# Kernel tuning notes

Measured on AMD Instinct MI355X. Metric: run time of the kernel, lower is better.

The kernel has to match this reference:

```python
import jax, jax.numpy as jnp
import numpy as np

N_NODES = 100000
N_EDGES = 1600000
IN_DIM, HID_DIM, OUT_DIM = 128, 256, 1


def setup_inputs() -> dict:
    key = jax.random.key(0)
    ks = jax.random.split(key, 8)
    x = jax.random.normal(ks[0], (N_NODES, IN_DIM), dtype=jnp.float32)
    edge_index = jax.random.randint(ks[1], (2, N_EDGES), 0, N_NODES, dtype=jnp.int64)
    # Glorot-ish scaled params (values arbitrary; shapes match GCNConv/Linear)
    W1 = jax.random.normal(ks[2], (IN_DIM, HID_DIM), dtype=jnp.float32) / np.sqrt(IN_DIM)
    b1 = jnp.zeros((HID_DIM,), dtype=jnp.float32)
    W2 = jax.random.normal(ks[3], (HID_DIM, HID_DIM), dtype=jnp.float32) / np.sqrt(HID_DIM)
    b2 = jnp.zeros((HID_DIM,), dtype=jnp.float32)
    Wout = jax.random.normal(ks[4], (HID_DIM, OUT_DIM), dtype=jnp.float32) / np.sqrt(HID_DIM)
    bout = jnp.zeros((OUT_DIM,), dtype=jnp.float32)
    return {"x": x, "edge_index": edge_index, "W1": W1, "b1": b1,
            "W2": W2, "b2": b2, "Wout": Wout, "bout": bout}


def _gcn_norm(edge_index, num_nodes):
    # add self loops, compute symmetric normalization deg^-1/2[src]*deg^-1/2[dst]
    loops = jnp.arange(num_nodes, dtype=edge_index.dtype)
    src = jnp.concatenate([edge_index[0], loops])
    dst = jnp.concatenate([edge_index[1], loops])
    deg = jax.ops.segment_sum(jnp.ones_like(dst, dtype=jnp.float32), dst,
                              num_segments=num_nodes)
    dinv = jnp.where(deg > 0, jax.lax.rsqrt(deg), 0.0)
    norm = dinv[src] * dinv[dst]  # [E + N]
    return src, dst, norm


def _gcn_layer(x, src, dst, norm, W, b, num_nodes):
    h = x @ W                                   # [N, F_out] dense transform
    msg = h[src] * norm[:, None]                # gather + scale  [E', F_out]
    agg = jax.ops.segment_sum(msg, dst, num_segments=num_nodes)  # scatter-add
    return agg + b


def reference(x, edge_index, W1, b1, W2, b2, Wout, bout):
    n = x.shape[0]
    src, dst, norm = _gcn_norm(edge_index, n)
    h = jax.nn.relu(_gcn_layer(x, src, dst, norm, W1, b1, n))
    h = jax.nn.relu(_gcn_layer(h, src, dst, norm, W2, b2, n))
    pooled = jnp.mean(h, axis=0, keepdims=True)  # global_mean_pool, one graph -> [1, H]
    return pooled @ Wout + bout                  # [1, 1]
```

## Files before the change

kernel.cpp:

```cpp
#include <hip/hip_runtime.h>
#include <hip/hip_bf16.h>


typedef __attribute__((ext_vector_type(8))) short short8;
typedef __attribute__((ext_vector_type(4))) float f32x4;
typedef __attribute__((ext_vector_type(2))) float f32x2;

#define BKT_SHIFT 9
#define BKT_NODES 512
#define BIN_CHUNK 8192
#define CAP 10240

__device__ inline unsigned short f2bf(float f) {
    union { float f; unsigned u; } v; v.f = f;
    unsigned r = (v.u + 0x7fff + ((v.u >> 16) & 1)) >> 16;
    return (unsigned short)r;
}

__global__ void init_k(int* __restrict__ bcur, float* __restrict__ pool, int NB) {
    int t = blockIdx.x * 256 + threadIdx.x;
    if (t < NB) bcur[t] = t * CAP;
    if (t < 256) pool[t] = 0.f;
}

__global__ __launch_bounds__(256) void bin_k(const int* __restrict__ ei,
                                             int* __restrict__ bcur,
                                             uint2* __restrict__ pairs,
                                             int E, int N, int NB) {
    __shared__ int hist[256];
    __shared__ int base[256];
    int chunk0 = blockIdx.x * BIN_CHUNK;
    for (int t = threadIdx.x; t < NB; t += 256) hist[t] = 0;
    __syncthreads();
#pragma unroll 4
    for (int i = 0; i < BIN_CHUNK / 256; ++i) {
        int e = chunk0 + i * 256 + threadIdx.x;
        if (e < E) {
            unsigned d = (unsigned)ei[(size_t)E + e];
            if (d < (unsigned)N) atomicAdd(&hist[d >> BKT_SHIFT], 1);
        }
    }
    __syncthreads();
    for (int t = threadIdx.x; t < NB; t += 256) {
        int c = hist[t];
        base[t] = c ? atomicAdd(&bcur[t], c) : 0;
        hist[t] = 0;
    }
    __syncthreads();
#pragma unroll 4
    for (int i = 0; i < BIN_CHUNK / 256; ++i) {
        int e = chunk0 + i * 256 + threadIdx.x;
        if (e < E) {
            unsigned d = (unsigned)ei[(size_t)E + e];
            unsigned s = (unsigned)ei[e];
            if (d < (unsigned)N) {
                int b = d >> BKT_SHIFT;
                int r = atomicAdd(&hist[b], 1);
                unsigned sc = (s < (unsigned)N) ? s : 0u;
                pairs[base[b] + r] = make_uint2(sc, d);
            }
        }
    }
}

__global__ __launch_bounds__(512) void scatter_k(const uint2* __restrict__ pairs,
                                                 const int* __restrict__ bcur,
                                                 int* __restrict__ off,
                                                 int* __restrict__ deg,
                                                 float* __restrict__ dinv,
                                                 int* __restrict__ csr, int N) {
    __shared__ int h[2][512];
    __shared__ int cur[512];
    int b = blockIdx.x, t = threadIdx.x;
    int lo = b << BKT_SHIFT;
    int rs = b * CAP;
    int re = min(bcur[b], rs + CAP);
    h[0][t] = 0;
    __syncthreads();
    for (int i = rs + t; i < re; i += 512)
        atomicAdd(&h[0][pairs[i].y - lo], 1);
    __syncthreads();
    int v = h[0][t];
    int cu = 0;
    for (int o = 1; o < 512; o <<= 1) {
        int val = h[cu][t];
        if (t >= o) val += h[cu][t - o];
        h[cu ^ 1][t] = val;
        cu ^= 1;
        __syncthreads();
    }
    int no = rs + (h[cu][t] - v);
    if (lo + t < N) {
        off[lo + t] = no;
        deg[lo + t] = v;
        dinv[lo + t] = rsqrtf((float)v + 1.0f);
    }
    cur[t] = no;
    __syncthreads();
    for (int i = rs + t; i < re; i += 512) {
        uint2 p = pairs[i];
        int pos = atomicAdd(&cur[p.y - lo], 1);
        csr[pos] = (int)p.x;
    }
}

__global__ void cvtx_k(const float* __restrict__ x, const float* __restrict__ dinv,
                       unsigned* __restrict__ Xs, int n32) {
    int idx = blockIdx.x * 256 + threadIdx.x;
    if (idx >= n32) return;
    int i = idx >> 5;
    float4 v = ((const float4*)x)[idx];
    float di = dinv[i];
    float a = fminf(fmaxf(di * v.x, -448.f), 448.f);
    float b = fminf(fmaxf(di * v.y, -448.f), 448.f);
    float c = fminf(fmaxf(di * v.z, -448.f), 448.f);
    float d = fminf(fmaxf(di * v.w, -448.f), 448.f);
    int p = __builtin_amdgcn_cvt_pk_fp8_f32(a, b, 0, false);
    p = __builtin_amdgcn_cvt_pk_fp8_f32(c, d, p, true);
    Xs[idx] = (unsigned)p;
}

__global__ void wt_k(const float* __restrict__ W, unsigned short* __restrict__ Wt, int K) {
    int idx = blockIdx.x * 256 + threadIdx.x;
    if (idx >= K * 256) return;
    int k = idx >> 8, nn = idx & 255;
    Wt[nn * K + k] = f2bf(W[idx]);
}

__global__ __launch_bounds__(256) void agg128_k(const unsigned short* __restrict__ X8,
                                                const int* __restrict__ csr,
                                                const int* __restrict__ off,
                                                const int* __restrict__ deg,
                                                const float* __restrict__ dinv,
                                                unsigned short* __restrict__ O8, int n) {
    int w = (blockIdx.x * 256 + threadIdx.x) >> 6;
    int lane = threadIdx.x & 63;
    if (w >= n) return;
    int st = off[w], c = deg[w];
    float di = dinv[w];
    f32x2 sv = __builtin_amdgcn_cvt_pk_f32_fp8((int)X8[(size_t)w * 64 + lane], false);
    float ax[4], ay[4];
    ax[0] = sv[0]; ay[0] = sv[1];
    ax[1] = ax[2] = ax[3] = 0.f; ay[1] = ay[2] = ay[3] = 0.f;
    int e = 0;
    for (; e + 8 <= c; e += 8) {
        int s[8];
#pragma unroll
        for (int j = 0; j < 8; ++j) s[j] = csr[st + e + j];
        unsigned short u[8];
#pragma unroll
        for (int j = 0; j < 8; ++j) u[j] = X8[(size_t)s[j] * 64 + lane];
#pragma unroll
        for (int j = 0; j < 8; ++j) {
            f32x2 f = __builtin_amdgcn_cvt_pk_f32_fp8((int)u[j], false);
            ax[j & 3] += f[0]; ay[j & 3] += f[1];
        }
    }
    if (e + 4 <= c) {
        int s[4];
#pragma unroll
        for (int j = 0; j < 4; ++j) s[j] = csr[st + e + j];
        unsigned short u[4];
#pragma unroll
        for (int j = 0; j < 4; ++j) u[j] = X8[(size_t)s[j] * 64 + lane];
#pragma unroll
        for (int j = 0; j < 4; ++j) {
            f32x2 f = __builtin_amdgcn_cvt_pk_f32_fp8((int)u[j], false);
            ax[j] += f[0]; ay[j] += f[1];
        }
        e += 4;
    }
    for (; e < c; ++e) {
        int s = csr[st + e];
        f32x2 f = __builtin_amdgcn_cvt_pk_f32_fp8((int)X8[(size_t)s * 64 + lane], false);
        ax[0] += f[0]; ay[0] += f[1];
    }
    float ox = di * ((ax[0] + ax[1]) + (ax[2] + ax[3]));
    float oy = di * ((ay[0] + ay[1]) + (ay[2] + ay[3]));
    ox = fminf(fmaxf(ox, -448.f), 448.f);
    oy = fminf(fmaxf(oy, -448.f), 448.f);
    int pk = __builtin_amdgcn_cvt_pk_fp8_f32(ox, oy, 0, false);
    O8[(size_t)w * 64 + lane] = (unsigned short)(pk & 0xffff);
}

__global__ __launch_bounds__(256) void agg256_k(const unsigned* __restrict__ H8,
                                                const int* __restrict__ csr,
                                                const int* __restrict__ off,
                                                const int* __restrict__ deg,
                                                const float* __restrict__ dinv,
                                                unsigned* __restrict__ O8, int n) {
    int w = (blockIdx.x * 256 + threadIdx.x) >> 6;
    int lane = threadIdx.x & 63;
    if (w >= n) return;
    int st = off[w], c = deg[w];
    float di = dinv[w];
    unsigned su = H8[(size_t)w * 64 + lane];
    f32x2 slo = __builtin_amdgcn_cvt_pk_f32_fp8((int)su, false);
    f32x2 shi = __builtin_amdgcn_cvt_pk_f32_fp8((int)su, true);
    float a[4][4];
    a[0][0] = slo[0]; a[0][1] = slo[1]; a[0][2] = shi[0]; a[0][3] = shi[1];
#pragma unroll
    for (int g = 1; g < 4; ++g) { a[g][0] = a[g][1] = a[g][2] = a[g][3] = 0.f; }
    int e = 0;
    for (; e + 8 <= c; e += 8) {
        int s[8];
#pragma unroll
        for (int j = 0; j < 8; ++j) s[j] = csr[st + e + j];
        unsigned u[8];
#pragma unroll
        for (int j = 0; j < 8; ++j) u[j] = H8[(size_t)s[j] * 64 + lane];
#pragma unroll
        for (int j = 0; j < 8; ++j) {
            f32x2 lo = __builtin_amdgcn_cvt_pk_f32_fp8((int)u[j], false);
            f32x2 hi = __builtin_amdgcn_cvt_pk_f32_fp8((int)u[j], true);
            a[j & 3][0] += lo[0]; a[j & 3][1] += lo[1];
            a[j & 3][2] += hi[0]; a[j & 3][3] += hi[1];
        }
    }
    if (e + 4 <= c) {
        int s[4];
#pragma unroll
        for (int j = 0; j < 4; ++j) s[j] = csr[st + e + j];
        unsigned u[4];
#pragma unroll
        for (int j = 0; j < 4; ++j) u[j] = H8[(size_t)s[j] * 64 + lane];
#pragma unroll
        for (int j = 0; j < 4; ++j) {
            f32x2 lo = __builtin_amdgcn_cvt_pk_f32_fp8((int)u[j], false);
            f32x2 hi = __builtin_amdgcn_cvt_pk_f32_fp8((int)u[j], true);
            a[j][0] += lo[0]; a[j][1] += lo[1]; a[j][2] += hi[0]; a[j][3] += hi[1];
        }
        e += 4;
    }
    for (; e < c; ++e) {
        int s = csr[st + e];
        unsigned u = H8[(size_t)s * 64 + lane];
        f32x2 lo = __builtin_amdgcn_cvt_pk_f32_fp8((int)u, false);
        f32x2 hi = __builtin_amdgcn_cvt_pk_f32_fp8((int)u, true);
        a[0][0] += lo[0]; a[0][1] += lo[1]; a[0][2] += hi[0]; a[0][3] += hi[1];
    }
    float o0 = di * ((a[0][0] + a[1][0]) + (a[2][0] + a[3][0]));
    float o1 = di * ((a[0][1] + a[1][1]) + (a[2][1] + a[3][1]));
    float o2 = di * ((a[0][2] + a[1][2]) + (a[2][2] + a[3][2]));
    float o3 = di * ((a[0][3] + a[1][3]) + (a[2][3] + a[3][3]));
    o0 = fminf(fmaxf(o0, -448.f), 448.f);
    o1 = fminf(fmaxf(o1, -448.f), 448.f);
    o2 = fminf(fmaxf(o2, -448.f), 448.f);
    o3 = fminf(fmaxf(o3, -448.f), 448.f);
    int pk = __builtin_amdgcn_cvt_pk_fp8_f32(o0, o1, 0, false);
    pk = __builtin_amdgcn_cvt_pk_fp8_f32(o2, o3, pk, true);
    O8[(size_t)w * 64 + lane] = (unsigned)pk;
}

template <int MODE>
__global__ __launch_bounds__(256) void mgemm_k(const unsigned char* __restrict__ A8,
                                               const unsigned short* __restrict__ Bt,
                                               const float* __restrict__ bias,
                                               const float* __restrict__ dinv,
                                               unsigned char* __restrict__ Hout8,
                                               float* __restrict__ pool,
                                               int M, int K) {
    __shared__ __align__(16) short As[64 * 40];
    __shared__ __align__(16) short Bs[256 * 40];
    int tid = threadIdx.x;
    int w = tid >> 6, lane = tid & 63, lr = lane >> 4, lc = lane & 15;
    int row0 = blockIdx.x * 64;
    int arow = tid >> 2, akoff = (tid & 3) * 8;
    f32x4 acc[16] = {};

    for (int kt = 0; kt < K; kt += 32) {
        short8 va = {};
        int gr = row0 + arow;
        if (gr < M) {
            uint2 v = *(const uint2*)(A8 + (size_t)gr * K + kt + akoff);
            f32x2 f0 = __builtin_amdgcn_cvt_pk_f32_fp8((int)v.x, false);
            f32x2 f1 = __builtin_amdgcn_cvt_pk_f32_fp8((int)v.x, true);
            f32x2 f2 = __builtin_amdgcn_cvt_pk_f32_fp8((int)v.y, false);
            f32x2 f3 = __builtin_amdgcn_cvt_pk_f32_fp8((int)v.y, true);
            va[0] = (short)f2bf(f0[0]); va[1] = (short)f2bf(f0[1]);
            va[2] = (short)f2bf(f1[0]); va[3] = (short)f2bf(f1[1]);
            va[4] = (short)f2bf(f2[0]); va[5] = (short)f2bf(f2[1]);
            va[6] = (short)f2bf(f3[0]); va[7] = (short)f2bf(f3[1]);
        }
        *(short8*)&As[arow * 40 + akoff] = va;
#pragma unroll
        for (int l = 0; l < 4; ++l) {
            int f = tid + l * 256;
            int br = f >> 2, bk = (f & 3) * 8;
            short8 vb = *(const short8*)(Bt + (size_t)br * K + kt + bk);
            *(short8*)&Bs[br * 40 + bk] = vb;
        }
        __syncthreads();
        short8 af = *(const short8*)&As[(w * 16 + lc) * 40 + lr * 8];
#pragma unroll
        for (int f = 0; f < 16; ++f) {
            short8 bf = *(const short8*)&Bs[(f * 16 + lc) * 40 + lr * 8];
            acc[f] = __builtin_amdgcn_mfma_f32_16x16x32_bf16(af, bf, acc[f], 0, 0, 0);
        }
        __syncthreads();
    }

    float bv[16];
#pragma unroll
    for (int f = 0; f < 16; ++f) bv[f] = bias[f * 16 + lc];

    if (MODE == 1) {
#pragma unroll
        for (int r = 0; r < 4; ++r) {
            int gr = row0 + w * 16 + lr * 4 + r;
            if (gr < M) {
                float dr = dinv[gr];
#pragma unroll
                for (int f = 0; f < 16; ++f) {
                    float v = fminf(dr * fmaxf(acc[f][r] + bv[f], 0.f), 448.f);
                    int p = __builtin_amdgcn_cvt_pk_fp8_f32(v, v, 0, false);
                    Hout8[(size_t)gr * 256 + f * 16 + lc] = (unsigned char)(p & 0xff);
                }
            }
        }
    } else {
        __shared__ float red[16][256];
        float s[16];
#pragma unroll
        for (int f = 0; f < 16; ++f) s[f] = 0.f;
#pragma unroll
        for (int r = 0; r < 4; ++r) {
            int gr = row0 + w * 16 + lr * 4 + r;
            if (gr < M) {
#pragma unroll
                for (int f = 0; f < 16; ++f)
                    s[f] += fmaxf(acc[f][r] + bv[f], 0.f);
            }
        }
#pragma unroll
        for (int f = 0; f < 16; ++f) red[w * 4 + lr][f * 16 + lc] = s[f];
        __syncthreads();
        float t = 0.f;
#pragma unroll
        for (int rr = 0; rr < 16; ++rr) t += red[rr][tid];
        atomicAdd(&pool[tid], t);
    }
}

__global__ void final_k(const float* __restrict__ pool, const float* __restrict__ Wout,
                        const float* __restrict__ bout, float* __restrict__ out, float invM) {
    __shared__ float s[256];
    int t = threadIdx.x;
    s[t] = pool[t] * invM * Wout[t];
    __syncthreads();
    for (int o = 128; o > 0; o >>= 1) {
        if (t < o) s[t] += s[t + o];
        __syncthreads();
    }
    if (t == 0) out[0] = s[0] + bout[0];
}

extern "C" void kernel_launch(void* const* d_in, const int* in_sizes, int n_in,
                              void* d_out, int out_size, void* d_ws, size_t ws_size,
                              hipStream_t stream) {
    const float* x    = (const float*)d_in[0];
    const int*   ei   = (const int*)d_in[1];
    const float* W1   = (const float*)d_in[2];
    const float* b1   = (const float*)d_in[3];
    const float* W2   = (const float*)d_in[4];
    const float* b2   = (const float*)d_in[5];
    const float* Wout = (const float*)d_in[6];
    const float* bout = (const float*)d_in[7];
    float* out = (float*)d_out;

    const int N = in_sizes[0] / 128;
    const int E = in_sizes[1] / 2;
    const int NB = (N + BKT_NODES - 1) / BKT_NODES;

    char* p = (char*)d_ws;
    auto carve = [&](size_t bytes) -> void* {
        void* r = (void*)p;
        p += (bytes + 511) & ~(size_t)511;
        return r;
    };
    unsigned*       Xs   = (unsigned*)carve((size_t)N * 128);
    unsigned short* Xp   = (unsigned short*)carve((size_t)N * 128);
    unsigned char*  H1   = (unsigned char*)carve((size_t)N * 256);
    unsigned*       G    = (unsigned*)carve((size_t)N * 256);
    unsigned short* Wt1  = (unsigned short*)carve((size_t)128 * 256 * 2);
    unsigned short* Wt2  = (unsigned short*)carve((size_t)256 * 256 * 2);
    float* dinv   = (float*)carve((size_t)N * 4);
    int*   off    = (int*)carve((size_t)N * 4);
    int*   deg    = (int*)carve((size_t)N * 4);
    int*   csr    = (int*)carve((size_t)NB * CAP * 4);
    uint2* pairs  = (uint2*)carve((size_t)NB * CAP * 8);
    int*   bcur   = (int*)carve((size_t)NB * 4);
    float* pool   = (float*)carve(256 * 4);

    init_k<<<1, 256, 0, stream>>>(bcur, pool, NB);
    bin_k<<<(E + BIN_CHUNK - 1) / BIN_CHUNK, 256, 0, stream>>>(ei, bcur, pairs, E, N, NB);
    scatter_k<<<NB, 512, 0, stream>>>(pairs, bcur, off, deg, dinv, csr, N);

    cvtx_k<<<(N * 32 + 255) / 256, 256, 0, stream>>>(x, dinv, Xs, N * 32);
    wt_k<<<(128 * 256 + 255) / 256, 256, 0, stream>>>(W1, Wt1, 128);
    wt_k<<<(256 * 256 + 255) / 256, 256, 0, stream>>>(W2, Wt2, 256);

    agg128_k<<<(N + 3) / 4, 256, 0, stream>>>((const unsigned short*)Xs, csr, off, deg, dinv, Xp, N);
    mgemm_k<1><<<(N + 63) / 64, 256, 0, stream>>>(
        (const unsigned char*)Xp, Wt1, b1, dinv, H1, nullptr, N, 128);

    agg256_k<<<(N + 3) / 4, 256, 0, stream>>>((const unsigned*)H1, csr, off, deg, dinv, G, N);
    mgemm_k<2><<<(N + 63) / 64, 256, 0, stream>>>(
        (const unsigned char*)G, Wt2, b2, nullptr, nullptr, pool, N, 256);

    final_k<<<1, 256, 0, stream>>>(pool, Wout, bout, out, 1.0f / N);
}
```

Measured before the change: 279.5 us.

## Fuse edge binning, x conversion and weight transposes into one prep kernel

Edge binning, fp8 conversion of x and both weight transposes now run as one multi-role kernel. To allow this, the x conversion no longer applies dinv, since dinv is only known after scatter. Instead the first aggregation multiplies each gathered neighbor by its own dinv, which adds a per-edge scalar gather. The bucket size is halved to 256 nodes with a smaller capacity, giving more scatter blocks, and init_k is replaced by memsets. This removes launches and the serial dependency of the conversion on scatter, at the cost of extra per-edge loads and fp8 quantization of unscaled x.

```diff
diff --git a/kernel.cpp b/kernel.cpp
--- a/kernel.cpp
+++ b/kernel.cpp
@@ -6,10 +6,10 @@
 typedef __attribute__((ext_vector_type(4))) float f32x4;
 typedef __attribute__((ext_vector_type(2))) float f32x2;
 
-#define BKT_SHIFT 9
-#define BKT_NODES 512
+#define BKT_SHIFT 8
+#define BKT_NODES 256
 #define BIN_CHUNK 8192
-#define CAP 10240
+#define CAP 4608
 
 __device__ inline unsigned short f2bf(float f) {
     union { float f; unsigned u; } v; v.f = f;
@@ -17,49 +17,74 @@
     return (unsigned short)r;
 }
 
-__global__ void init_k(int* __restrict__ bcur, float* __restrict__ pool, int NB) {
-    int t = blockIdx.x * 256 + threadIdx.x;
-    if (t < NB) bcur[t] = t * CAP;
-    if (t < 256) pool[t] = 0.f;
-}
-
-__global__ __launch_bounds__(256) void bin_k(const int* __restrict__ ei,
-                                             int* __restrict__ bcur,
-                                             uint2* __restrict__ pairs,
-                                             int E, int N, int NB) {
-    __shared__ int hist[256];
-    __shared__ int base[256];
-    int chunk0 = blockIdx.x * BIN_CHUNK;
-    for (int t = threadIdx.x; t < NB; t += 256) hist[t] = 0;
-    __syncthreads();
+__global__ __launch_bounds__(256) void prep_k(const int* __restrict__ ei,
+                                              int* __restrict__ bcur,
+                                              uint2* __restrict__ pairs,
+                                              const float* __restrict__ x,
+                                              unsigned* __restrict__ Xs,
+                                              const float* __restrict__ W1,
+                                              unsigned short* __restrict__ Wt1,
+                                              const float* __restrict__ W2,
+                                              unsigned short* __restrict__ Wt2,
+                                              int E, int N, int NB,
+                                              int NCHUNK, int NCVT) {
+    int b = blockIdx.x;
+    int tid = threadIdx.x;
+    if (b < NCHUNK) {
+        __shared__ int hist[512];
+        __shared__ int base[512];
+        int chunk0 = b * BIN_CHUNK;
+        for (int t = tid; t < NB; t += 256) hist[t] = 0;
+        __syncthreads();
 #pragma unroll 4
-    for (int i = 0; i < BIN_CHUNK / 256; ++i) {
-        int e = chunk0 + i * 256 + threadIdx.x;
-        if (e < E) {
-            unsigned d = (unsigned)ei[(size_t)E + e];
-            if (d < (unsigned)N) atomicAdd(&hist[d >> BKT_SHIFT], 1);
-        }
-    }
-    __syncthreads();
-    for (int t = threadIdx.x; t < NB; t += 256) {
-        int c = hist[t];
-        base[t] = c ? atomicAdd(&bcur[t], c) : 0;
-        hist[t] = 0;
-    }
-    __syncthreads();
+        for (int i = 0; i < BIN_CHUNK / 256; ++i) {
+            int e = chunk0 + i * 256 + tid;
+            if (e < E) {
+                unsigned d = (unsigned)ei[(size_t)E + e];
+                if (d < (unsigned)N) atomicAdd(&hist[d >> BKT_SHIFT], 1);
+            }
+        }
+        __syncthreads();
+        for (int t = tid; t < NB; t += 256) {
+            int c = hist[t];
+            base[t] = c ? (t * CAP + atomicAdd(&bcur[t], c)) : 0;
+            hist[t] = 0;
+        }
+        __syncthreads();
 #pragma unroll 4
-    for (int i = 0; i < BIN_CHUNK / 256; ++i) {
-        int e = chunk0 + i * 256 + threadIdx.x;
-        if (e < E) {
-            unsigned d = (unsigned)ei[(size_t)E + e];
-            unsigned s = (unsigned)ei[e];
-            if (d < (unsigned)N) {
-                int b = d >> BKT_SHIFT;
-                int r = atomicAdd(&hist[b], 1);
-                unsigned sc = (s < (unsigned)N) ? s : 0u;
-                pairs[base[b] + r] = make_uint2(sc, d);
+        for (int i = 0; i < BIN_CHUNK / 256; ++i) {
+            int e = chunk0 + i * 256 + tid;
+            if (e < E) {
+                unsigned d = (unsigned)ei[(size_t)E + e];
+                unsigned s = (unsigned)ei[e];
+                if (d < (unsigned)N) {
+                    int bb = d >> BKT_SHIFT;
+                    int r = atomicAdd(&hist[bb], 1);
+                    unsigned sc = (s < (unsigned)N) ? s : 0u;
+                    pairs[base[bb] + r] = make_uint2(sc, d);
+                }
             }
         }
+    } else if (b < NCHUNK + NCVT) {
+        int idx = (b - NCHUNK) * 256 + tid;
+        if (idx < N * 32) {
+            float4 v = ((const float4*)x)[idx];
+            float a = fminf(fmaxf(v.x, -448.f), 448.f);
+            float bb = fminf(fmaxf(v.y, -448.f), 448.f);
+            float c = fminf(fmaxf(v.z, -448.f), 448.f);
+            float d = fminf(fmaxf(v.w, -448.f), 448.f);
+            int p = __builtin_amdgcn_cvt_pk_fp8_f32(a, bb, 0, false);
+            p = __builtin_amdgcn_cvt_pk_fp8_f32(c, d, p, true);
+            Xs[idx] = (unsigned)p;
+        }
+    } else if (b < NCHUNK + NCVT + 128) {
+        int idx = (b - NCHUNK - NCVT) * 256 + tid;
+        int k = idx >> 8, nn = idx & 255;
+        Wt1[nn * 128 + k] = f2bf(W1[idx]);
+    } else {
+        int idx = (b - NCHUNK - NCVT - 128) * 256 + tid;
+        int k = idx >> 8, nn = idx & 255;
+        Wt2[nn * 256 + k] = f2bf(W2[idx]);
     }
 }
 
@@ -69,62 +94,42 @@
                                                  int* __restrict__ deg,
                                                  float* __restrict__ dinv,
                                                  int* __restrict__ csr, int N) {
-    __shared__ int h[2][512];
-    __shared__ int cur[512];
+    __shared__ int h[2][256];
+    __shared__ int cur[256];
     int b = blockIdx.x, t = threadIdx.x;
     int lo = b << BKT_SHIFT;
     int rs = b * CAP;
-    int re = min(bcur[b], rs + CAP);
-    h[0][t] = 0;
+    int re = rs + min(bcur[b], CAP);
+    if (t < 256) h[0][t] = 0;
     __syncthreads();
     for (int i = rs + t; i < re; i += 512)
         atomicAdd(&h[0][pairs[i].y - lo], 1);
     __syncthreads();
-    int v = h[0][t];
+    int v = (t < 256) ? h[0][t] : 0;
     int cu = 0;
-    for (int o = 1; o < 512; o <<= 1) {
-        int val = h[cu][t];
-        if (t >= o) val += h[cu][t - o];
-        h[cu ^ 1][t] = val;
+    for (int o = 1; o < 256; o <<= 1) {
+        int val = 0;
+        if (t < 256) { val = h[cu][t]; if (t >= o) val += h[cu][t - o]; }
+        __syncthreads();
+        if (t < 256) h[cu ^ 1][t] = val;
         cu ^= 1;
         __syncthreads();
     }
-    int no = rs + (h[cu][t] - v);
-    if (lo + t < N) {
-        off[lo + t] = no;
-        deg[lo + t] = v;
-        dinv[lo + t] = rsqrtf((float)v + 1.0f);
-    }
-    cur[t] = no;
+    if (t < 256) {
+        int no = rs + (h[cu][t] - v);
+        if (lo + t < N) {
+            off[lo + t] = no;
+            deg[lo + t] = v;
+            dinv[lo + t] = rsqrtf((float)v + 1.0f);
+        }
+        cur[t] = no;
+    }
     __syncthreads();
     for (int i = rs + t; i < re; i += 512) {
         uint2 p = pairs[i];
         int pos = atomicAdd(&cur[p.y - lo], 1);
         csr[pos] = (int)p.x;
     }
-}
-
-__global__ void cvtx_k(const float* __restrict__ x, const float* __restrict__ dinv,
-                       unsigned* __restrict__ Xs, int n32) {
-    int idx = blockIdx.x * 256 + threadIdx.x;
-    if (idx >= n32) return;
-    int i = idx >> 5;
-    float4 v = ((const float4*)x)[idx];
-    float di = dinv[i];
-    float a = fminf(fmaxf(di * v.x, -448.f), 448.f);
-    float b = fminf(fmaxf(di * v.y, -448.f), 448.f);
-    float c = fminf(fmaxf(di * v.z, -448.f), 448.f);
-    float d = fminf(fmaxf(di * v.w, -448.f), 448.f);
-    int p = __builtin_amdgcn_cvt_pk_fp8_f32(a, b, 0, false);
-    p = __builtin_amdgcn_cvt_pk_fp8_f32(c, d, p, true);
-    Xs[idx] = (unsigned)p;
-}
-
-__global__ void wt_k(const float* __restrict__ W, unsigned short* __restrict__ Wt, int K) {
-    int idx = blockIdx.x * 256 + threadIdx.x;
-    if (idx >= K * 256) return;
-    int k = idx >> 8, nn = idx & 255;
-    Wt[nn * K + k] = f2bf(W[idx]);
 }
 
 __global__ __launch_bounds__(256) void agg128_k(const unsigned short* __restrict__ X8,
@@ -140,40 +145,47 @@
     float di = dinv[w];
     f32x2 sv = __builtin_amdgcn_cvt_pk_f32_fp8((int)X8[(size_t)w * 64 + lane], false);
     float ax[4], ay[4];
-    ax[0] = sv[0]; ay[0] = sv[1];
+    ax[0] = di * sv[0]; ay[0] = di * sv[1];
     ax[1] = ax[2] = ax[3] = 0.f; ay[1] = ay[2] = ay[3] = 0.f;
     int e = 0;
     for (; e + 8 <= c; e += 8) {
         int s[8];
 #pragma unroll
         for (int j = 0; j < 8; ++j) s[j] = csr[st + e + j];
+        float wd[8];
+#pragma unroll
+        for (int j = 0; j < 8; ++j) wd[j] = dinv[s[j]];
         unsigned short u[8];
 #pragma unroll
         for (int j = 0; j < 8; ++j) u[j] = X8[(size_t)s[j] * 64 + lane];
 #pragma unroll
         for (int j = 0; j < 8; ++j) {
             f32x2 f = __builtin_amdgcn_cvt_pk_f32_fp8((int)u[j], false);
-            ax[j & 3] += f[0]; ay[j & 3] += f[1];
+            ax[j & 3] += wd[j] * f[0]; ay[j & 3] += wd[j] * f[1];
         }
     }
     if (e + 4 <= c) {
         int s[4];
 #pragma unroll
         for (int j = 0; j < 4; ++j) s[j] = csr[st + e + j];
+        float wd[4];
+#pragma unroll
+        for (int j = 0; j < 4; ++j) wd[j] = dinv[s[j]];
         unsigned short u[4];
 #pragma unroll
         for (int j = 0; j < 4; ++j) u[j] = X8[(size_t)s[j] * 64 + lane];
 #pragma unroll
         for (int j = 0; j < 4; ++j) {
             f32x2 f = __builtin_amdgcn_cvt_pk_f32_fp8((int)u[j], false);
-            ax[j] += f[0]; ay[j] += f[1];
+            ax[j] += wd[j] * f[0]; ay[j] += wd[j] * f[1];
         }
         e += 4;
     }
     for (; e < c; ++e) {
         int s = csr[st + e];
+        float wd = dinv[s];
         f32x2 f = __builtin_amdgcn_cvt_pk_f32_fp8((int)X8[(size_t)s * 64 + lane], false);
-        ax[0] += f[0]; ay[0] += f[1];
+        ax[0] += wd * f[0]; ay[0] += wd * f[1];
     }
     float ox = di * ((ax[0] + ax[1]) + (ax[2] + ax[3]));
     float oy = di * ((ay[0] + ay[1]) + (ay[2] + ay[3]));
@@ -371,6 +383,8 @@
     const int N = in_sizes[0] / 128;
     const int E = in_sizes[1] / 2;
     const int NB = (N + BKT_NODES - 1) / BKT_NODES;
+    const int NCHUNK = (E + BIN_CHUNK - 1) / BIN_CHUNK;
+    const int NCVT = (N * 32 + 255) / 256;
 
     char* p = (char*)d_ws;
     auto carve = [&](size_t bytes) -> void* {
@@ -392,13 +406,12 @@
     int*   bcur   = (int*)carve((size_t)NB * 4);
     float* pool   = (float*)carve(256 * 4);
 
-    init_k<<<1, 256, 0, stream>>>(bcur, pool, NB);
-    bin_k<<<(E + BIN_CHUNK - 1) / BIN_CHUNK, 256, 0, stream>>>(ei, bcur, pairs, E, N, NB);
+    hipMemsetAsync(bcur, 0, (size_t)NB * 4, stream);
+    hipMemsetAsync(pool, 0, 256 * 4, stream);
+
+    prep_k<<<NCHUNK + NCVT + 128 + 256, 256, 0, stream>>>(
+        ei, bcur, pairs, x, Xs, W1, Wt1, W2, Wt2, E, N, NB, NCHUNK, NCVT);
     scatter_k<<<NB, 512, 0, stream>>>(pairs, bcur, off, deg, dinv, csr, N);
-
-    cvtx_k<<<(N * 32 + 255) / 256, 256, 0, stream>>>(x, dinv, Xs, N * 32);
-    wt_k<<<(128 * 256 + 255) / 256, 256, 0, stream>>>(W1, Wt1, 128);
-    wt_k<<<(256 * 256 + 255) / 256, 256, 0, stream>>>(W2, Wt2, 256);
 
     agg128_k<<<(N + 3) / 4, 256, 0, stream>>>((const unsigned short*)Xs, csr, off, deg, dinv, Xp, N);
     mgemm_k<1><<<(N + 63) / 64, 256, 0, stream>>>(
```

Result: no change. 278.2 us (-0.5%).
